# Optimization experiments

Measured on AMD Instinct MI355X. Metric: run time of the kernel, lower is better.

Reference implementation:

```python
import jax, jax.numpy as jnp
import numpy as np
import math

NFEAT = 1024
NHID = 512
NLAYERS = 8
LAMDA = 0.5
ALPHA = 0.1
N_DIA = 48
DIA_L = 64
N = N_DIA * DIA_L


def setup_inputs() -> dict:
    key = jax.random.key(0)
    ks = jax.random.split(key, 16)
    stdv_fc = 1.0 / math.sqrt(NFEAT)
    stdv_gc = 1.0 / math.sqrt(NHID)
    inp = {
        'a': jax.random.normal(ks[0], (N, NFEAT), jnp.float32),
        'v': jax.random.normal(ks[1], (N, NFEAT), jnp.float32),
        'l': jax.random.normal(ks[2], (N, NFEAT), jnp.float32),
        'W0': jax.random.uniform(ks[3], (NFEAT, NHID), jnp.float32, -stdv_fc, stdv_fc),
        'b0': jax.random.uniform(ks[4], (NHID,), jnp.float32, -stdv_fc, stdv_fc),
        'W1': jax.random.uniform(ks[5], (NFEAT, NHID), jnp.float32, -stdv_fc, stdv_fc),
        'b1': jax.random.uniform(ks[6], (NHID,), jnp.float32, -stdv_fc, stdv_fc),
        'W2': jax.random.uniform(ks[7], (NFEAT, NHID), jnp.float32, -stdv_fc, stdv_fc),
        'b2': jax.random.uniform(ks[8], (NHID,), jnp.float32, -stdv_fc, stdv_fc),
        'Wconv': jax.random.uniform(ks[9], (NLAYERS, NHID, NHID), jnp.float32, -stdv_gc, stdv_gc),
        'dia_len': DIA_L,  # uniform dialogue length
        'topicLabel': jnp.zeros((N,), jnp.int64),
    }
    return inp


def create_big_adj(a, v, l, dia_l):
    n = a.shape[0]
    d = n // dia_l
    feats = jnp.stack([a, v, l])                    # [3, N, F]
    x = feats.reshape(3, d, dia_l, -1)              # [3, D, L, F]
    nrm = x / jnp.sqrt(jnp.sum(x * x, axis=-1, keepdims=True))
    cos = jnp.einsum('mdif,mdjf->mdij', nrm, nrm) * 0.99999
    sim = jnp.arccos(cos)                           # [3, D, L, L]
    adj = jnp.zeros((3 * n, 3 * n), dtype=a.dtype)
    base = jnp.arange(d)[:, None, None] * dia_l     # dialogue start offsets
    rows = jnp.broadcast_to(base + jnp.arange(dia_l)[:, None], (d, dia_l, dia_l))
    cols = jnp.broadcast_to(base + jnp.arange(dia_l)[None, :], (d, dia_l, dia_l))
    for m in range(3):  # same-modality block-diagonal acos-similarity blocks
        adj = adj.at[m * n + rows, m * n + cols].set(sim[m])
    k = jnp.arange(n)
    for m in range(3):  # cross-modal: same-utterance links set to 0.99999
        for mm in range(3):
            if m != mm:
                adj = adj.at[m * n + k, mm * n + k].set(0.99999)
    dsum = jnp.sum(adj, axis=1)
    dinv = dsum ** -0.5
    return dinv[:, None] * adj * dinv[None, :]


def reference(a, v, l, W0, b0, W1, b1, W2, b2, Wconv, dia_len, topicLabel):
    relu = jax.nn.relu
    # eval mode: dropout is identity
    a_ = relu(a @ W0 + b0)
    l_ = relu(l @ W1 + b1)
    v_ = relu(v @ W2 + b2)
    x = jnp.concatenate([a_, v_, l_], axis=0)       # [3N, nhidden]
    adj = create_big_adj(a, v, l, dia_len)
    h0 = x
    h = x
    for i in range(NLAYERS):
        theta = math.log(LAMDA / (i + 1) + 1.0)
        hi = adj @ h
        support = (1.0 - ALPHA) * hi + ALPHA * h0
        h = relu(theta * (support @ Wconv[i]) + (1.0 - theta) * support)
    n = a.shape[0]
    out = jnp.concatenate([h[:n], h[n:2 * n], h[2 * n:]], axis=-1)  # [N, 3*nhidden]
    out = jnp.concatenate([l, out], axis=-1)        # use_residue
    return out
```

## Files before the change

kernel.cpp:

```cpp
#include <hip/hip_runtime.h>
#include <hip/hip_bf16.h>
#include <cmath>

#define NFEAT 1024
#define NHID  512
#define NLAYERS 8
#define NDIA 48
#define DIAL 64
#define NROW (NDIA*DIAL)
#define NROW3 (3*NROW)

typedef short bf16x8 __attribute__((ext_vector_type(8)));
typedef float f32x4  __attribute__((ext_vector_type(4)));
typedef unsigned short u16x8 __attribute__((ext_vector_type(8)));
typedef unsigned short u16x4 __attribute__((ext_vector_type(4)));
typedef unsigned short ushort_t;

__device__ __forceinline__ unsigned short f2bf(float x) {
  __hip_bfloat16 h = __float2bfloat16(x);
  return __builtin_bit_cast(unsigned short, h);
}
__device__ __forceinline__ float bf2f(unsigned short u) {
  __hip_bfloat16 h = __builtin_bit_cast(__hip_bfloat16, u);
  return __bfloat162float(h);
}

__device__ __forceinline__ void gload16(const void* g, void* l) {
  __builtin_amdgcn_global_load_lds(
      (const __attribute__((address_space(1))) void*)g,
      (__attribute__((address_space(3))) void*)l, 16, 0, 0);
}

__global__ __launch_bounds__(256) void k_prep(const float* __restrict__ a, const float* __restrict__ v,
                      const float* __restrict__ l, ushort_t* __restrict__ Abuf,
                      ushort_t* __restrict__ Xn) {
  int gid = blockIdx.x * 256 + threadIdx.x;
  int row = gid >> 6, lane = gid & 63;
  int m = row / NROW, r = row % NROW;
  const float* src = (m == 0 ? a : (m == 1 ? v : l)) + (size_t)r * NFEAT;
  float4 x[4];
  float s = 0.f;
#pragma unroll
  for (int q = 0; q < 4; ++q) {
    x[q] = *reinterpret_cast<const float4*>(src + lane * 4 + q * 256);
    s += x[q].x*x[q].x + x[q].y*x[q].y + x[q].z*x[q].z + x[q].w*x[q].w;
  }
#pragma unroll
  for (int off = 32; off; off >>= 1) s += __shfl_xor(s, off);
  float inv = rsqrtf(s);
  ushort_t* da = Abuf + (size_t)row * NFEAT;
  ushort_t* dn = Xn + (size_t)row * NFEAT;
#pragma unroll
  for (int q = 0; q < 4; ++q) {
    u16x4 oa, on;
    oa[0] = f2bf(x[q].x); oa[1] = f2bf(x[q].y); oa[2] = f2bf(x[q].z); oa[3] = f2bf(x[q].w);
    on[0] = f2bf(x[q].x * inv); on[1] = f2bf(x[q].y * inv);
    on[2] = f2bf(x[q].z * inv); on[3] = f2bf(x[q].w * inv);
    *reinterpret_cast<u16x4*>(da + lane * 4 + q * 256) = oa;
    *reinterpret_cast<u16x4*>(dn + lane * 4 + q * 256) = on;
  }
}

__global__ __launch_bounds__(256) void k_simm(const ushort_t* __restrict__ Xn,
                      ushort_t* __restrict__ Sbf, float* __restrict__ dinv) {
  __shared__ short Xs[2][4096];
  __shared__ float simS[64][73];
  int blk = blockIdx.x;
  const ushort_t* Xb = Xn + (size_t)blk * 64 * NFEAT;
  int t = threadIdx.x, w = t >> 6, lane = t & 63;
  f32x4 acc[4] = {};

#define STAGE_SIM(b, k0) do { \
    _Pragma("unroll") \
    for (int q = 0; q < 2; ++q) { \
      int f_ = t * 8 + q * 2048; \
      int row_ = f_ >> 6; \
      int col_ = (f_ & 63) ^ ((row_ & 7) << 3); \
      gload16(Xb + (size_t)row_ * NFEAT + (k0) + col_, (void*)(Xs[b] + q * 2048 + w * 512)); \
    } } while (0)

  STAGE_SIM(0, 0);
  __syncthreads();
  for (int it = 0; it < 16; ++it) {
    int cur = it & 1;
    if (it < 15) STAGE_SIM(cur ^ 1, (it + 1) * 64);
    const char* base = (const char*)Xs[cur];
#pragma unroll
    for (int ks = 0; ks < 2; ++ks) {
      int koff = ks * 32 + (lane >> 4) * 8;
      int arow = w * 16 + (lane & 15);
      bf16x8 af = *(const bf16x8*)(base + (((arow << 7) + (koff << 1)) ^ ((arow & 7) << 4)));
#pragma unroll
      for (int j = 0; j < 4; ++j) {
        int brow = j * 16 + (lane & 15);
        bf16x8 bf = *(const bf16x8*)(base + (((brow << 7) + (koff << 1)) ^ ((brow & 7) << 4)));
        acc[j] = __builtin_amdgcn_mfma_f32_16x16x32_bf16(af, bf, acc[j], 0, 0, 0);
      }
    }
    __syncthreads();
  }
#undef STAGE_SIM

#pragma unroll
  for (int j = 0; j < 4; ++j)
#pragma unroll
    for (int e = 0; e < 4; ++e) {
      int r = w * 16 + (lane >> 4) * 4 + e;
      int c = j * 16 + (lane & 15);
      float cc = acc[j][e] * 0.99999f;
      cc = fminf(fmaxf(cc, -0.99999f), 0.99999f);
      simS[r][c] = acosf(cc);
    }
  __syncthreads();
  if (t < 64) {
    float s = 0.f;
#pragma unroll 8
    for (int c = 0; c < 64; ++c) s += simS[t][c];
    float di = rsqrtf(s + 1.99998f);
    simS[t][64] = di;
    dinv[blk * 64 + t] = di;
  }
  __syncthreads();
  ushort_t* Sb = Sbf + (size_t)blk * 4096;
#pragma unroll
  for (int q = 0; q < 2; ++q) {
    int idx = t * 8 + q * 2048;
    int i = idx >> 6, j0 = idx & 63;
    float di = simS[i][64];
    u16x8 o;
#pragma unroll
    for (int e = 0; e < 8; ++e)
      o[e] = f2bf(simS[i][j0 + e] * di * simS[j0 + e][64]);
    *reinterpret_cast<u16x8*>(Sb + idx) = o;
  }
}

__global__ void k_cvt_w(const float* __restrict__ s0, const float* __restrict__ s1,
                        const float* __restrict__ s2, ushort_t* __restrict__ dst,
                        int K, int mode) {
  __shared__ float tile[32][33];
  int z = blockIdx.z;
  const float* src = (mode == 1) ? (s0 + (size_t)z * K * NHID)
                                 : (z == 0 ? s0 : (z == 1 ? s1 : s2));
  ushort_t* d = dst + (size_t)z * NHID * K;
  int n0 = blockIdx.x * 32, k0 = blockIdx.y * 32;
  int tx = threadIdx.x & 31, ty = threadIdx.x >> 5;
#pragma unroll
  for (int q = 0; q < 4; ++q)
    tile[ty + q * 8][tx] = src[(size_t)(k0 + ty + q * 8) * NHID + n0 + tx];
  __syncthreads();
#pragma unroll
  for (int q = 0; q < 4; ++q)
    d[(size_t)(n0 + ty + q * 8) * K + k0 + tx] = f2bf(tile[tx][ty + q * 8]);
}

template<int EPI>
__global__ __launch_bounds__(256) void k_gemm_mfma(
    const ushort_t* __restrict__ A, const ushort_t* __restrict__ B,
    const float* __restrict__ ba, const float* __restrict__ bv, const float* __restrict__ bl,
    const ushort_t* __restrict__ sup, ushort_t* __restrict__ C, ushort_t* __restrict__ C2,
    int K, float theta) {
  __shared__ short As[2][128 * 64];
  __shared__ short Bs[2][64 * 64];
  int t = threadIdx.x;
  int w = t >> 6, lane = t & 63;
  int bm = blockIdx.x * 128, bn = blockIdx.y * 64;
  const float* bias = ba;
  if (EPI == 0) {
    int band = bm / NROW;
    B += (size_t)band * NHID * K;
    bias = (band == 0 ? ba : (band == 1 ? bv : bl));
  }
  const ushort_t* Ab = A + (size_t)bm * K;
  const ushort_t* Bb = B + (size_t)bn * K;
  int wr = (w >> 1) * 64, wc = (w & 1) * 32;
  f32x4 acc[4][2] = {};

#define STAGE_G(b, k0) do { \
    _Pragma("unroll") \
    for (int q = 0; q < 4; ++q) { \
      int f_ = t * 8 + q * 2048; int row_ = f_ >> 6; \
      int col_ = (f_ & 63) ^ ((row_ & 7) << 3); \
      gload16(Ab + (size_t)row_ * K + (k0) + col_, (void*)(As[b] + q * 2048 + w * 512)); } \
    _Pragma("unroll") \
    for (int q = 0; q < 2; ++q) { \
      int f_ = t * 8 + q * 2048; int row_ = f_ >> 6; \
      int col_ = (f_ & 63) ^ ((row_ & 7) << 3); \
      gload16(Bb + (size_t)row_ * K + (k0) + col_, (void*)(Bs[b] + q * 2048 + w * 512)); } \
  } while (0)

  STAGE_G(0, 0);
  __syncthreads();
  int T = K >> 6;
  for (int s = 0; s < T; ++s) {
    int cur = s & 1;
    if (s + 1 < T) STAGE_G(cur ^ 1, (s + 1) * 64);
    const char* ab = (const char*)As[cur];
    const char* bb = (const char*)Bs[cur];
#pragma unroll
    for (int ks = 0; ks < 2; ++ks) {
      bf16x8 af[4], bfr[2];
#pragma unroll
      for (int i = 0; i < 4; ++i) {
        int arow = wr + i * 16 + (lane & 15);
        int abo = (arow << 7) + ((ks * 32 + (lane >> 4) * 8) << 1);
        af[i] = *reinterpret_cast<const bf16x8*>(ab + (abo ^ ((arow & 7) << 4)));
      }
#pragma unroll
      for (int j = 0; j < 2; ++j) {
        int brow = wc + j * 16 + (lane & 15);
        int bbo = (brow << 7) + ((ks * 32 + (lane >> 4) * 8) << 1);
        bfr[j] = *reinterpret_cast<const bf16x8*>(bb + (bbo ^ ((brow & 7) << 4)));
      }
#pragma unroll
      for (int i = 0; i < 4; ++i)
#pragma unroll
        for (int j = 0; j < 2; ++j)
          acc[i][j] = __builtin_amdgcn_mfma_f32_16x16x32_bf16(af[i], bfr[j], acc[i][j], 0, 0, 0);
    }
    __syncthreads();
  }
#undef STAGE_G

#pragma unroll
  for (int i = 0; i < 4; ++i) {
#pragma unroll
    for (int jf = 0; jf < 2; ++jf) {
      int r0 = bm + wr + i * 16 + (lane >> 4) * 4;
      int c  = bn + wc + jf * 16 + (lane & 15);
#pragma unroll
      for (int j = 0; j < 4; ++j) {
        int r = r0 + j;
        float val = acc[i][jf][j];
        if (EPI == 0) {
          val = fmaxf(val + bias[c], 0.f);
          unsigned short o = f2bf(val);
          C[(size_t)r * NHID + c] = o;
          C2[(size_t)r * NHID + c] = o;
        } else {
          float s = bf2f(sup[(size_t)r * NHID + c]);
          val = fmaxf(theta * val + (1.f - theta) * s, 0.f);
          C[(size_t)r * NHID + c] = f2bf(val);
        }
      }
    }
  }
}

__global__ __launch_bounds__(256) void k_adj(const ushort_t* __restrict__ Sbf,
                      const ushort_t* __restrict__ h, const ushort_t* __restrict__ h0,
                      const float* __restrict__ dinv, ushort_t* __restrict__ sup) {
  __shared__ short Ss[3 * 4096];
  __shared__ short Ht[3][64][72];
  __shared__ float supS[64][69];
  int d = blockIdx.x, c0 = blockIdx.y * 64;
  int t = threadIdx.x, w = t >> 6, lane = t & 63;
#pragma unroll
  for (int q = 0; q < 6; ++q) {
    int f = t * 8 + q * 2048;
    int mod = f >> 12, rem = f & 4095;
    int row = rem >> 6;
    int col = (rem & 63) ^ ((row & 7) << 3);
    gload16(Sbf + ((size_t)(mod * NDIA + d)) * 4096 + row * 64 + col,
            (void*)(Ss + q * 2048 + w * 512));
  }
#pragma unroll
  for (int q = 0; q < 6; ++q) {
    int idx = t + q * 256;
    int mod = idx >> 9, rem = idx & 511;
    int j = rem >> 3, n0 = (rem & 7) * 8;
    int key = rem & 7;
    u16x8 hv = *reinterpret_cast<const u16x8*>(
        h + ((size_t)(mod * NROW + d * 64 + j)) * NHID + c0 + n0);
    int js = j ^ (key << 3);
#pragma unroll
    for (int e = 0; e < 8; ++e) Ht[mod][n0 + e][js] = hv[e];
  }
  __syncthreads();
  f32x4 acc[3][4] = {};
#pragma unroll
  for (int m = 0; m < 3; ++m)
#pragma unroll
    for (int ks = 0; ks < 2; ++ks) {
      int koff = ks * 32 + (lane >> 4) * 8;
      int arow = w * 16 + (lane & 15);
      bf16x8 af = *(const bf16x8*)((const char*)Ss + m * 8192 +
                    (((arow << 7) + (koff << 1)) ^ ((arow & 7) << 4)));
#pragma unroll
      for (int j = 0; j < 4; ++j) {
        int n = j * 16 + (lane & 15);
        int koff_s = koff ^ (((n >> 3) & 7) << 3);
        bf16x8 bf = *(const bf16x8*)(&Ht[m][n][koff_s]);
        acc[m][j] = __builtin_amdgcn_mfma_f32_16x16x32_bf16(af, bf, acc[m][j], 0, 0, 0);
      }
    }
  int r = t >> 2, cc0 = (t & 3) * 16;
  int u = d * 64 + r;
  float d0 = dinv[u], d1 = dinv[NROW + u], d2 = dinv[2 * NROW + u];
  float dv[3] = {d0, d1, d2};
  for (int m = 0; m < 3; ++m) {
#pragma unroll
    for (int j = 0; j < 4; ++j)
#pragma unroll
      for (int e = 0; e < 4; ++e)
        supS[w * 16 + (lane >> 4) * 4 + e][j * 16 + (lane & 15)] = acc[m][j][e];
    __syncthreads();
    int mm1 = (m + 1) % 3, mm2 = (m + 2) % 3;
    int g = m * NROW + u;
    float c1 = 0.99999f * dv[m] * dv[mm1];
    float c2 = 0.99999f * dv[m] * dv[mm2];
    const ushort_t* p1 = h + ((size_t)(mm1 * NROW + u)) * NHID + c0 + cc0;
    const ushort_t* p2 = h + ((size_t)(mm2 * NROW + u)) * NHID + c0 + cc0;
    const ushort_t* pz = h0 + (size_t)g * NHID + c0 + cc0;
    ushort_t* po = sup + (size_t)g * NHID + c0 + cc0;
#pragma unroll
    for (int half = 0; half < 2; ++half) {
      u16x8 h1 = *reinterpret_cast<const u16x8*>(p1 + half * 8);
      u16x8 h2 = *reinterpret_cast<const u16x8*>(p2 + half * 8);
      u16x8 hz = *reinterpret_cast<const u16x8*>(pz + half * 8);
      u16x8 o;
#pragma unroll
      for (int e = 0; e < 8; ++e) {
        float val = 0.9f * (supS[r][cc0 + half * 8 + e] + c1 * bf2f(h1[e]) + c2 * bf2f(h2[e]))
                  + 0.1f * bf2f(hz[e]);
        o[e] = f2bf(val);
      }
      *reinterpret_cast<u16x8*>(po + half * 8) = o;
    }
    __syncthreads();
  }
}

__global__ void k_out(const float* __restrict__ l, const ushort_t* __restrict__ h,
                      float* __restrict__ out) {
  int idx = blockIdx.x * blockDim.x + threadIdx.x;
  int i = idx / 640;
  int c4 = (idx % 640) * 4;
  float4 val;
  if (c4 < 1024) {
    val = *reinterpret_cast<const float4*>(l + (size_t)i * NFEAT + c4);
  } else {
    int cc = c4 - 1024;
    int m = cc >> 9, c = cc & 511;
    u16x4 hv = *reinterpret_cast<const u16x4*>(h + ((size_t)m * NROW + i) * NHID + c);
    val.x = bf2f(hv[0]); val.y = bf2f(hv[1]); val.z = bf2f(hv[2]); val.w = bf2f(hv[3]);
  }
  *reinterpret_cast<float4*>(out + (size_t)i * 2560 + c4) = val;
}

extern "C" void kernel_launch(void* const* d_in, const int* in_sizes, int n_in,
                              void* d_out, int out_size, void* d_ws, size_t ws_size,
                              hipStream_t stream) {
  const float* a  = (const float*)d_in[0];
  const float* v  = (const float*)d_in[1];
  const float* l  = (const float*)d_in[2];
  const float* W0 = (const float*)d_in[3];
  const float* b0 = (const float*)d_in[4];
  const float* W1 = (const float*)d_in[5];
  const float* b1 = (const float*)d_in[6];
  const float* W2 = (const float*)d_in[7];
  const float* b2 = (const float*)d_in[8];
  const float* Wc = (const float*)d_in[9];
  float* out = (float*)d_out;

  const size_t SZ = (size_t)NROW3 * NHID;
  const size_t XSZ = (size_t)3 * NROW * NFEAT;
  char* ws = (char*)d_ws;
  ushort_t* Abuf = (ushort_t*)ws;  ws += XSZ * 2;
  ushort_t* Xn   = (ushort_t*)ws;  ws += XSZ * 2;
  ushort_t* h0   = (ushort_t*)ws;  ws += SZ * 2;
  ushort_t* Wtfc = (ushort_t*)ws;  ws += (size_t)3 * NHID * NFEAT * 2;
  ushort_t* Wct  = (ushort_t*)ws;  ws += (size_t)NLAYERS * NHID * NHID * 2;
  ushort_t* Sbf  = (ushort_t*)ws;  ws += (size_t)144 * 4096 * 2;
  float* dinv    = (float*)ws;
  ushort_t* h   = Xn;
  ushort_t* sup = Xn + SZ;

  k_prep<<<NROW3 / 4, 256, 0, stream>>>(a, v, l, Abuf, Xn);
  k_cvt_w<<<dim3(NHID / 32, NFEAT / 32, 3), 256, 0, stream>>>(W0, W2, W1, Wtfc, NFEAT, 0);
  k_cvt_w<<<dim3(NHID / 32, NHID / 32, NLAYERS), 256, 0, stream>>>(Wc, nullptr, nullptr, Wct, NHID, 1);
  k_simm<<<3 * NDIA, 256, 0, stream>>>(Xn, Sbf, dinv);

  k_gemm_mfma<0><<<dim3(NROW3 / 128, NHID / 64), 256, 0, stream>>>(
      Abuf, Wtfc, b0, b2, b1, nullptr, h0, h, NFEAT, 0.f);

  for (int i = 0; i < NLAYERS; ++i) {
    float theta = (float)std::log(0.5 / (i + 1) + 1.0);
    k_adj<<<dim3(NDIA, NHID / 64), 256, 0, stream>>>(Sbf, h, h0, dinv, sup);
    k_gemm_mfma<1><<<dim3(NROW3 / 128, NHID / 64), 256, 0, stream>>>(
        sup, Wct + (size_t)i * NHID * NHID, nullptr, nullptr, nullptr, sup, h, nullptr, NHID, theta);
  }

  k_out<<<(NROW * 2560 / 4) / 256, 256, 0, stream>>>(l, h, out);
}
```

Measured before the change: 235.0 us.

## Drop normalized bf16 copy; apply row norms in similarity epilogue and restructure adj LDS

```diff
diff --git a/kernel.cpp b/kernel.cpp
--- a/kernel.cpp
+++ b/kernel.cpp
@@ -33,7 +33,7 @@
 
 __global__ __launch_bounds__(256) void k_prep(const float* __restrict__ a, const float* __restrict__ v,
                       const float* __restrict__ l, ushort_t* __restrict__ Abuf,
-                      ushort_t* __restrict__ Xn) {
+                      float* __restrict__ invn) {
   int gid = blockIdx.x * 256 + threadIdx.x;
   int row = gid >> 6, lane = gid & 63;
   int m = row / NROW, r = row % NROW;
@@ -47,27 +47,26 @@
   }
 #pragma unroll
   for (int off = 32; off; off >>= 1) s += __shfl_xor(s, off);
-  float inv = rsqrtf(s);
+  if (lane == 0) invn[row] = rsqrtf(s);
   ushort_t* da = Abuf + (size_t)row * NFEAT;
-  ushort_t* dn = Xn + (size_t)row * NFEAT;
 #pragma unroll
   for (int q = 0; q < 4; ++q) {
-    u16x4 oa, on;
+    u16x4 oa;
     oa[0] = f2bf(x[q].x); oa[1] = f2bf(x[q].y); oa[2] = f2bf(x[q].z); oa[3] = f2bf(x[q].w);
-    on[0] = f2bf(x[q].x * inv); on[1] = f2bf(x[q].y * inv);
-    on[2] = f2bf(x[q].z * inv); on[3] = f2bf(x[q].w * inv);
     *reinterpret_cast<u16x4*>(da + lane * 4 + q * 256) = oa;
-    *reinterpret_cast<u16x4*>(dn + lane * 4 + q * 256) = on;
-  }
-}
-
-__global__ __launch_bounds__(256) void k_simm(const ushort_t* __restrict__ Xn,
+  }
+}
+
+__global__ __launch_bounds__(256) void k_simm(const ushort_t* __restrict__ Ab,
+                      const float* __restrict__ invn,
                       ushort_t* __restrict__ Sbf, float* __restrict__ dinv) {
   __shared__ short Xs[2][4096];
   __shared__ float simS[64][73];
+  __shared__ float invS[64];
   int blk = blockIdx.x;
-  const ushort_t* Xb = Xn + (size_t)blk * 64 * NFEAT;
+  const ushort_t* Xb = Ab + (size_t)blk * 64 * NFEAT;
   int t = threadIdx.x, w = t >> 6, lane = t & 63;
+  if (t < 64) invS[t] = invn[blk * 64 + t];
   f32x4 acc[4] = {};
 
 #define STAGE_SIM(b, k0) do { \
@@ -107,7 +106,7 @@
     for (int e = 0; e < 4; ++e) {
       int r = w * 16 + (lane >> 4) * 4 + e;
       int c = j * 16 + (lane & 15);
-      float cc = acc[j][e] * 0.99999f;
+      float cc = acc[j][e] * invS[r] * invS[c] * 0.99999f;
       cc = fminf(fmaxf(cc, -0.99999f), 0.99999f);
       simS[r][c] = acosf(cc);
     }
@@ -250,9 +249,10 @@
 __global__ __launch_bounds__(256) void k_adj(const ushort_t* __restrict__ Sbf,
                       const ushort_t* __restrict__ h, const ushort_t* __restrict__ h0,
                       const float* __restrict__ dinv, ushort_t* __restrict__ sup) {
-  __shared__ short Ss[3 * 4096];
-  __shared__ short Ht[3][64][72];
-  __shared__ float supS[64][69];
+  __shared__ char ldsb[52224];
+  short* Ss = (short*)ldsb;
+  short (*Ht)[72] = (short (*)[72])(ldsb + 24576);
+  float (*supF)[68] = (float (*)[68])ldsb;
   int d = blockIdx.x, c0 = blockIdx.y * 64;
   int t = threadIdx.x, w = t >> 6, lane = t & 63;
 #pragma unroll
@@ -274,7 +274,7 @@
         h + ((size_t)(mod * NROW + d * 64 + j)) * NHID + c0 + n0);
     int js = j ^ (key << 3);
 #pragma unroll
-    for (int e = 0; e < 8; ++e) Ht[mod][n0 + e][js] = hv[e];
+    for (int e = 0; e < 8; ++e) Ht[mod * 64 + n0 + e][js] = hv[e];
   }
   __syncthreads();
   f32x4 acc[3][4] = {};
@@ -290,21 +290,24 @@
       for (int j = 0; j < 4; ++j) {
         int n = j * 16 + (lane & 15);
         int koff_s = koff ^ (((n >> 3) & 7) << 3);
-        bf16x8 bf = *(const bf16x8*)(&Ht[m][n][koff_s]);
+        bf16x8 bf = *(const bf16x8*)(&Ht[m * 64 + n][koff_s]);
         acc[m][j] = __builtin_amdgcn_mfma_f32_16x16x32_bf16(af, bf, acc[m][j], 0, 0, 0);
       }
     }
+  __syncthreads();
+#pragma unroll
+  for (int m = 0; m < 3; ++m)
+#pragma unroll
+    for (int j = 0; j < 4; ++j)
+#pragma unroll
+      for (int e = 0; e < 4; ++e)
+        supF[m * 64 + w * 16 + (lane >> 4) * 4 + e][j * 16 + (lane & 15)] = acc[m][j][e];
+  __syncthreads();
   int r = t >> 2, cc0 = (t & 3) * 16;
   int u = d * 64 + r;
-  float d0 = dinv[u], d1 = dinv[NROW + u], d2 = dinv[2 * NROW + u];
-  float dv[3] = {d0, d1, d2};
+  float dv[3] = {dinv[u], dinv[NROW + u], dinv[2 * NROW + u]};
+#pragma unroll
   for (int m = 0; m < 3; ++m) {
-#pragma unroll
-    for (int j = 0; j < 4; ++j)
-#pragma unroll
-      for (int e = 0; e < 4; ++e)
-        supS[w * 16 + (lane >> 4) * 4 + e][j * 16 + (lane & 15)] = acc[m][j][e];
-    __syncthreads();
     int mm1 = (m + 1) % 3, mm2 = (m + 2) % 3;
     int g = m * NROW + u;
     float c1 = 0.99999f * dv[m] * dv[mm1];
@@ -321,13 +324,13 @@
       u16x8 o;
 #pragma unroll
       for (int e = 0; e < 8; ++e) {
-        float val = 0.9f * (supS[r][cc0 + half * 8 + e] + c1 * bf2f(h1[e]) + c2 * bf2f(h2[e]))
+        float val = 0.9f * (supF[m * 64 + r][cc0 + half * 8 + e]
+                    + c1 * bf2f(h1[e]) + c2 * bf2f(h2[e]))
                   + 0.1f * bf2f(hz[e]);
         o[e] = f2bf(val);
       }
       *reinterpret_cast<u16x8*>(po + half * 8) = o;
     }
-    __syncthreads();
   }
 }
 
@@ -367,19 +370,19 @@
   const size_t XSZ = (size_t)3 * NROW * NFEAT;
   char* ws = (char*)d_ws;
   ushort_t* Abuf = (ushort_t*)ws;  ws += XSZ * 2;
-  ushort_t* Xn   = (ushort_t*)ws;  ws += XSZ * 2;
   ushort_t* h0   = (ushort_t*)ws;  ws += SZ * 2;
+  ushort_t* h    = (ushort_t*)ws;  ws += SZ * 2;
+  ushort_t* sup  = (ushort_t*)ws;  ws += SZ * 2;
   ushort_t* Wtfc = (ushort_t*)ws;  ws += (size_t)3 * NHID * NFEAT * 2;
   ushort_t* Wct  = (ushort_t*)ws;  ws += (size_t)NLAYERS * NHID * NHID * 2;
   ushort_t* Sbf  = (ushort_t*)ws;  ws += (size_t)144 * 4096 * 2;
-  float* dinv    = (float*)ws;
-  ushort_t* h   = Xn;
-  ushort_t* sup = Xn + SZ;
-
-  k_prep<<<NROW3 / 4, 256, 0, stream>>>(a, v, l, Abuf, Xn);
+  float* dinv    = (float*)ws;     ws += (size_t)NROW3 * 4;
+  float* invn    = (float*)ws;
+
+  k_prep<<<NROW3 / 4, 256, 0, stream>>>(a, v, l, Abuf, invn);
   k_cvt_w<<<dim3(NHID / 32, NFEAT / 32, 3), 256, 0, stream>>>(W0, W2, W1, Wtfc, NFEAT, 0);
   k_cvt_w<<<dim3(NHID / 32, NHID / 32, NLAYERS), 256, 0, stream>>>(Wc, nullptr, nullptr, Wct, NHID, 1);
-  k_simm<<<3 * NDIA, 256, 0, stream>>>(Xn, Sbf, dinv);
+  k_simm<<<3 * NDIA, 256, 0, stream>>>(Abuf, invn, Sbf, dinv);
 
   k_gemm_mfma<0><<<dim3(NROW3 / 128, NHID / 64), 256, 0, stream>>>(
       Abuf, Wtfc, b0, b2, b1, nullptr, h0, h, NFEAT, 0.f);
```

Result: faster. 229.7 us (median of 2 runs) (-2.2%).
